# Kernel optimization log

Hardware: AMD Instinct MI355X
Metric: run time of the kernel (lower is better)

The kernel has to match this reference:

```python
import jax, jax.numpy as jnp
import numpy as np

TAU = 0.5
EPS = 1e-8
NEG = -1e30  # masked logit value (finite to keep grads clean)

B, L1, L2 = 8, 2048, 2048


def setup_inputs() -> dict:
    key = jax.random.key(0)
    k1, k2 = jax.random.split(key)
    sim_matrix = jax.random.normal(k1, (B, L1, L2), dtype=jnp.float32)
    # per-sample valid lengths in [1024, 2048] so masking is exercised but no row is empty
    lengths = jax.random.randint(k2, (B, 2), 1024, 2049, dtype=jnp.int32)
    return {"sim_matrix": sim_matrix, "lengths": lengths}


def reference(sim_matrix, lengths):
    # mask[b,i,j] = (i < lengths[b,0]) & (j < lengths[b,1])
    i_idx = jnp.arange(sim_matrix.shape[1])[None, :, None]
    j_idx = jnp.arange(sim_matrix.shape[2])[None, None, :]
    mask = (i_idx < lengths[:, 0, None, None]) & (j_idx < lengths[:, 1, None, None])

    logits = jnp.where(mask, sim_matrix / TAU, NEG)
    row_sm = jax.nn.softmax(logits, axis=-1)   # competition over L2 per row
    col_sm = jax.nn.softmax(logits, axis=-2)   # competition over L1 per column

    # geometric mean of the two assignments; zero outside valid region
    out = jnp.where(mask, jnp.sqrt(EPS + row_sm * col_sm), 0.0)
    return out
```

## Files before the change

### kernel.cpp

```cpp
#include <hip/hip_runtime.h>
#include <math.h>

#define L 2048
#define BATCH 8
#define RPS 32
#define NSPLIT (L / RPS)
#define EPSF 1e-8f
#define C2 2.885390081777927f
#define C4 5.770780163555854f

__device__ __forceinline__ float fexp2(float x) {
  return __builtin_amdgcn_exp2f(x);
}

__global__ __launch_bounds__(512) void stats_k(
    const float* __restrict__ sim, const int* __restrict__ lengths,
    float* __restrict__ rinv, float* __restrict__ pcol) {
  const int b = blockIdx.y;
  const int islab = blockIdx.x;
  const int len0 = lengths[2 * b], len1 = lengths[2 * b + 1];
  const int tid = threadIdx.x;
  const int j = tid * 4;
  const int i0 = islab * RPS;
  const int iend = min(i0 + RPS, len0);

  float4 msk;
  msk.x = (j + 0 < len1) ? 1.f : 0.f;
  msk.y = (j + 1 < len1) ? 1.f : 0.f;
  msk.z = (j + 2 < len1) ? 1.f : 0.f;
  msk.w = (j + 3 < len1) ? 1.f : 0.f;

  float4 cacc = make_float4(0.f, 0.f, 0.f, 0.f);
  __shared__ float rowpart[RPS][8];
  const int wave = tid >> 6, lane = tid & 63;

  const float* p = sim + ((size_t)b * L + i0) * L + j;
  for (int i = i0; i < iend; ++i, p += L) {
    float4 v = *reinterpret_cast<const float4*>(p);
    float4 e;
    e.x = fexp2(v.x * C2) * msk.x;
    e.y = fexp2(v.y * C2) * msk.y;
    e.z = fexp2(v.z * C2) * msk.z;
    e.w = fexp2(v.w * C2) * msk.w;
    cacc.x += e.x; cacc.y += e.y; cacc.z += e.z; cacc.w += e.w;
    float r = (e.x + e.y) + (e.z + e.w);
#pragma unroll
    for (int off = 1; off < 64; off <<= 1) r += __shfl_xor(r, off, 64);
    if (lane == 0) rowpart[i - i0][wave] = r;
  }
  __syncthreads();

  if (tid < RPS) {
    const int i = i0 + tid;
    if (i < len0) {
      float s = 0.f;
#pragma unroll
      for (int w = 0; w < 8; ++w) s += rowpart[tid][w];
      rinv[b * L + i] = 1.0f / s;
    }
  }
  const size_t o = (size_t)(b * NSPLIT + islab) * L + j;
  *reinterpret_cast<float4*>(pcol + o) = cacc;
}

__global__ __launch_bounds__(256) void col_merge_k(
    const float* __restrict__ pcol, float* __restrict__ cinv) {
  const int idx = blockIdx.x * 256 + threadIdx.x;
  const int b = idx >> 11, j = idx & (L - 1);
  const float* p = pcol + (size_t)b * NSPLIT * L + j;
  float s = 0.f;
#pragma unroll 8
  for (int c = 0; c < NSPLIT; ++c) s += p[(size_t)c * L];
  cinv[idx] = 1.0f / s;
}

__global__ __launch_bounds__(256) void finalize_k(
    const float* __restrict__ sim, const int* __restrict__ lengths,
    const float* __restrict__ rinv, const float* __restrict__ cinv,
    float* __restrict__ out) {
  const int row = blockIdx.y;
  const int b = row >> 11, i = row & (L - 1);
  const int len0 = lengths[2 * b], len1 = lengths[2 * b + 1];
  const int j = (blockIdx.x << 10) + threadIdx.x * 4;
  const size_t off = (size_t)row * L + j;
  float4 o;
  if (i >= len0) {
    o = make_float4(0.f, 0.f, 0.f, 0.f);
  } else {
    const float ri = rinv[row];
    float4 v = *reinterpret_cast<const float4*>(sim + off);
    float4 ci = *reinterpret_cast<const float4*>(cinv + (size_t)b * L + j);
    o.x = (j + 0 < len1) ? sqrtf(EPSF + fexp2(v.x * C4) * ri * ci.x) : 0.f;
    o.y = (j + 1 < len1) ? sqrtf(EPSF + fexp2(v.y * C4) * ri * ci.y) : 0.f;
    o.z = (j + 2 < len1) ? sqrtf(EPSF + fexp2(v.z * C4) * ri * ci.z) : 0.f;
    o.w = (j + 3 < len1) ? sqrtf(EPSF + fexp2(v.w * C4) * ri * ci.w) : 0.f;
  }
  *reinterpret_cast<float4*>(out + off) = o;
}

extern "C" void kernel_launch(void* const* d_in, const int* in_sizes, int n_in,
                              void* d_out, int out_size, void* d_ws, size_t ws_size,
                              hipStream_t stream) {
  const float* sim = (const float*)d_in[0];
  const int* lengths = (const int*)d_in[1];
  float* out = (float*)d_out;
  float* ws = (float*)d_ws;

  const int NR = BATCH * L;
  float* rinv = ws;
  float* cinv = ws + NR;
  float* pcol = ws + 2 * (size_t)NR;

  hipLaunchKernelGGL(stats_k, dim3(NSPLIT, BATCH), dim3(512), 0, stream,
                     sim, lengths, rinv, pcol);
  hipLaunchKernelGGL(col_merge_k, dim3(NR / 256), dim3(256), 0, stream,
                     pcol, cinv);
  hipLaunchKernelGGL(finalize_k, dim3(2, NR), dim3(256), 0, stream,
                     sim, lengths, rinv, cinv, out);
}
```

Before: 244.7 us.

## Restructure stats kernel to wave-per-row tiles with LDS column reduction

Each wave in the stats kernel now processes four full rows (2048 columns, eight float4 per lane). Row sums are reduced within the wave and written directly, which removes the per-row shared-memory row partials. Column partials from the four waves are combined through a 32 KB LDS buffer before a single store per slab. Slabs are halved to 16 rows, doubling the pcol partials that col_merge must read. col_merge and finalize launch geometries are also retuned, and the extra LDS and registers may lower occupancy.

Result: no change. 244.5 us (-0.1%).

```diff
diff --git a/kernel.cpp b/kernel.cpp
--- a/kernel.cpp
+++ b/kernel.cpp
@@ -3,7 +3,7 @@
 
 #define L 2048
 #define BATCH 8
-#define RPS 32
+#define RPS 16
 #define NSPLIT (L / RPS)
 #define EPSF 1e-8f
 #define C2 2.885390081777927f
@@ -13,75 +13,88 @@
   return __builtin_amdgcn_exp2f(x);
 }
 
-__global__ __launch_bounds__(512) void stats_k(
+__global__ __launch_bounds__(256) void stats_k(
     const float* __restrict__ sim, const int* __restrict__ lengths,
     float* __restrict__ rinv, float* __restrict__ pcol) {
   const int b = blockIdx.y;
   const int islab = blockIdx.x;
   const int len0 = lengths[2 * b], len1 = lengths[2 * b + 1];
   const int tid = threadIdx.x;
-  const int j = tid * 4;
-  const int i0 = islab * RPS;
-  const int iend = min(i0 + RPS, len0);
+  const int wave = tid >> 6, lane = tid & 63;
+  const int i0 = islab * RPS + wave * 4;
+  const int jb = lane * 4;
 
-  float4 msk;
-  msk.x = (j + 0 < len1) ? 1.f : 0.f;
-  msk.y = (j + 1 < len1) ? 1.f : 0.f;
-  msk.z = (j + 2 < len1) ? 1.f : 0.f;
-  msk.w = (j + 3 < len1) ? 1.f : 0.f;
+  float4 cacc[8];
+#pragma unroll
+  for (int s = 0; s < 8; ++s) cacc[s] = make_float4(0.f, 0.f, 0.f, 0.f);
 
-  float4 cacc = make_float4(0.f, 0.f, 0.f, 0.f);
-  __shared__ float rowpart[RPS][8];
-  const int wave = tid >> 6, lane = tid & 63;
+  for (int r = 0; r < 4; ++r) {
+    const int i = i0 + r;
+    if (i >= len0) break;
+    const float* p = sim + ((size_t)b * L + i) * L + jb;
+    float racc = 0.f;
+#pragma unroll
+    for (int s = 0; s < 8; ++s) {
+      float4 v = *reinterpret_cast<const float4*>(p + s * 256);
+      float4 e;
+      e.x = fexp2(v.x * C2); e.y = fexp2(v.y * C2);
+      e.z = fexp2(v.z * C2); e.w = fexp2(v.w * C2);
+      if (s >= 4) {
+        const int j = s * 256 + jb;
+        if (j + 0 >= len1) e.x = 0.f;
+        if (j + 1 >= len1) e.y = 0.f;
+        if (j + 2 >= len1) e.z = 0.f;
+        if (j + 3 >= len1) e.w = 0.f;
+      }
+      racc += (e.x + e.y) + (e.z + e.w);
+      cacc[s].x += e.x; cacc[s].y += e.y; cacc[s].z += e.z; cacc[s].w += e.w;
+    }
+#pragma unroll
+    for (int off = 1; off < 64; off <<= 1) racc += __shfl_xor(racc, off, 64);
+    if (lane == 0) rinv[(size_t)b * L + i] = 1.0f / racc;
+  }
 
-  const float* p = sim + ((size_t)b * L + i0) * L + j;
-  for (int i = i0; i < iend; ++i, p += L) {
-    float4 v = *reinterpret_cast<const float4*>(p);
-    float4 e;
-    e.x = fexp2(v.x * C2) * msk.x;
-    e.y = fexp2(v.y * C2) * msk.y;
-    e.z = fexp2(v.z * C2) * msk.z;
-    e.w = fexp2(v.w * C2) * msk.w;
-    cacc.x += e.x; cacc.y += e.y; cacc.z += e.z; cacc.w += e.w;
-    float r = (e.x + e.y) + (e.z + e.w);
+  __shared__ float cpart[4][2048];
 #pragma unroll
-    for (int off = 1; off < 64; off <<= 1) r += __shfl_xor(r, off, 64);
-    if (lane == 0) rowpart[i - i0][wave] = r;
-  }
+  for (int s = 0; s < 8; ++s)
+    *reinterpret_cast<float4*>(&cpart[wave][s * 256 + jb]) = cacc[s];
   __syncthreads();
 
-  if (tid < RPS) {
-    const int i = i0 + tid;
-    if (i < len0) {
-      float s = 0.f;
 #pragma unroll
-      for (int w = 0; w < 8; ++w) s += rowpart[tid][w];
-      rinv[b * L + i] = 1.0f / s;
-    }
+  for (int h = 0; h < 2; ++h) {
+    const int c = h * 1024 + tid * 4;
+    float4 a0 = *reinterpret_cast<const float4*>(&cpart[0][c]);
+    float4 a1 = *reinterpret_cast<const float4*>(&cpart[1][c]);
+    float4 a2 = *reinterpret_cast<const float4*>(&cpart[2][c]);
+    float4 a3 = *reinterpret_cast<const float4*>(&cpart[3][c]);
+    float4 o;
+    o.x = (a0.x + a1.x) + (a2.x + a3.x);
+    o.y = (a0.y + a1.y) + (a2.y + a3.y);
+    o.z = (a0.z + a1.z) + (a2.z + a3.z);
+    o.w = (a0.w + a1.w) + (a2.w + a3.w);
+    *reinterpret_cast<float4*>(&pcol[(size_t)(b * NSPLIT + islab) * L + c]) = o;
   }
-  const size_t o = (size_t)(b * NSPLIT + islab) * L + j;
-  *reinterpret_cast<float4*>(pcol + o) = cacc;
 }
 
-__global__ __launch_bounds__(256) void col_merge_k(
+__global__ __launch_bounds__(128) void col_merge_k(
     const float* __restrict__ pcol, float* __restrict__ cinv) {
-  const int idx = blockIdx.x * 256 + threadIdx.x;
+  const int idx = blockIdx.x * 128 + threadIdx.x;
   const int b = idx >> 11, j = idx & (L - 1);
   const float* p = pcol + (size_t)b * NSPLIT * L + j;
   float s = 0.f;
-#pragma unroll 8
+#pragma unroll 16
   for (int c = 0; c < NSPLIT; ++c) s += p[(size_t)c * L];
   cinv[idx] = 1.0f / s;
 }
 
-__global__ __launch_bounds__(256) void finalize_k(
+__global__ __launch_bounds__(512) void finalize_k(
     const float* __restrict__ sim, const int* __restrict__ lengths,
     const float* __restrict__ rinv, const float* __restrict__ cinv,
     float* __restrict__ out) {
-  const int row = blockIdx.y;
+  const int row = blockIdx.x;
   const int b = row >> 11, i = row & (L - 1);
   const int len0 = lengths[2 * b], len1 = lengths[2 * b + 1];
-  const int j = (blockIdx.x << 10) + threadIdx.x * 4;
+  const int j = threadIdx.x * 4;
   const size_t off = (size_t)row * L + j;
   float4 o;
   if (i >= len0) {
@@ -89,7 +102,7 @@
   } else {
     const float ri = rinv[row];
     float4 v = *reinterpret_cast<const float4*>(sim + off);
-    float4 ci = *reinterpret_cast<const float4*>(cinv + (size_t)b * L + j);
+    float4 ci = *reinterpret_cast<const float4*>(cinv + ((size_t)b << 11) + j);
     o.x = (j + 0 < len1) ? sqrtf(EPSF + fexp2(v.x * C4) * ri * ci.x) : 0.f;
     o.y = (j + 1 < len1) ? sqrtf(EPSF + fexp2(v.y * C4) * ri * ci.y) : 0.f;
     o.z = (j + 2 < len1) ? sqrtf(EPSF + fexp2(v.z * C4) * ri * ci.z) : 0.f;
@@ -111,10 +124,10 @@
   float* cinv = ws + NR;
   float* pcol = ws + 2 * (size_t)NR;
 
-  hipLaunchKernelGGL(stats_k, dim3(NSPLIT, BATCH), dim3(512), 0, stream,
+  hipLaunchKernelGGL(stats_k, dim3(NSPLIT, BATCH), dim3(256), 0, stream,
                      sim, lengths, rinv, pcol);
-  hipLaunchKernelGGL(col_merge_k, dim3(NR / 256), dim3(256), 0, stream,
+  hipLaunchKernelGGL(col_merge_k, dim3(NR / 128), dim3(128), 0, stream,
                      pcol, cinv);
-  hipLaunchKernelGGL(finalize_k, dim3(2, NR), dim3(256), 0, stream,
+  hipLaunchKernelGGL(finalize_k, dim3(NR), dim3(512), 0, stream,
                      sim, lengths, rinv, cinv, out);
 }
```
